# Optimization experiments

Hardware: AMD Instinct MI355X
Metric: run time of the kernel (lower is better)

Reference implementation:

```python
import jax, jax.numpy as jnp
import numpy as np

B, T, TF = 4, 16000, 80
NC, NR, NS, NO, NIN, NL = 80, 64, 256, 256, 256, 16
K_UP, STRIDE = 800, 200
LOOP_FACTOR = 8  # floor(log2(128)) + 1


def setup_inputs() -> dict:
    key = jax.random.key(0)
    ks = jax.random.split(key, 16)
    s = 0.05
    return {
        "features": jax.random.normal(ks[0], (B, NC, TF), jnp.float32),
        "forward_input": jax.random.randint(ks[1], (B, T), 0, NIN, jnp.int32),
        "embed_table": jax.random.normal(ks[2], (NIN, NR), jnp.float32) * s,
        "up_w": jax.random.normal(ks[3], (NC, NC, K_UP), jnp.float32) * s,  # torch ConvTranspose1d (in,out,K)
        "up_b": jnp.zeros((NC,), jnp.float32),
        "cond_w": jax.random.normal(ks[4], (2 * NR * NL, NC), jnp.float32) * s,
        "cond_b": jnp.zeros((2 * NR * NL,), jnp.float32),
        "dil_w": jax.random.normal(ks[5], (NL, 2 * NR, NR, 2), jnp.float32) * s,
        "dil_b": jnp.zeros((NL, 2 * NR), jnp.float32),
        "res_w": jax.random.normal(ks[6], (NL - 1, NR, NR), jnp.float32) * s,
        "res_b": jnp.zeros((NL - 1, NR), jnp.float32),
        "skip_w": jax.random.normal(ks[7], (NL, NS, NR), jnp.float32) * s,
        "skip_b": jnp.zeros((NL, NS), jnp.float32),
        "out_w": jax.random.normal(ks[8], (NO, NS), jnp.float32) * s,
        "end_w": jax.random.normal(ks[9], (NO, NO), jnp.float32) * s,
    }


def reference(features, forward_input, embed_table, up_w, up_b, cond_w, cond_b,
              dil_w, dil_b, res_w, res_b, skip_w, skip_b, out_w, end_w):
    # ConvTranspose1d(stride=200): conv with lhs_dilation, spatially-flipped kernel, in/out swapped
    k_t = jnp.flip(up_w, -1).transpose(1, 0, 2)  # (out, in, K)
    cond = jax.lax.conv_general_dilated(
        features, k_t, window_strides=(1,), padding=[(K_UP - 1, K_UP - 1)],
        lhs_dilation=(STRIDE,), dimension_numbers=('NCH', 'OIH', 'NCH'))
    cond = cond + up_b[None, :, None]
    cond = cond[:, :, :T]  # truncate to signal length

    x = embed_table[forward_input].transpose(0, 2, 1)  # [B, NR, T]

    cond_acts = jnp.einsum('oc,bct->bot', cond_w, cond) + cond_b[None, :, None]
    cond_acts = cond_acts.reshape(B, NL, 2 * NR, T)

    res_acts = None
    output = None
    for i in range(NL):
        d = 2 ** (i % LOOP_FACTOR)
        prev = jnp.pad(x, ((0, 0), (0, 0), (d, 0)))[:, :, :T]  # causal shift by dilation
        in_act = (jnp.einsum('oi,bit->bot', dil_w[i, :, :, 0], prev)
                  + jnp.einsum('oi,bit->bot', dil_w[i, :, :, 1], x)
                  + dil_b[i][None, :, None] + cond_acts[:, i])
        acts = jnp.tanh(in_act[:, :NR]) * jax.nn.sigmoid(in_act[:, NR:])
        if i < NL - 1:
            res_acts = jnp.einsum('oi,bit->bot', res_w[i], acts) + res_b[i][None, :, None]
        # NOTE: faithful to original: on last layer res_acts is stale (from layer NL-2)
        x = res_acts + x
        skip = jnp.einsum('oi,bit->bot', skip_w[i], acts) + skip_b[i][None, :, None]
        output = skip if output is None else output + skip

    output = jax.nn.relu(output)
    output = jax.nn.relu(jnp.einsum('os,bst->bot', out_w, output))
    output = jnp.einsum('oi,bit->bot', end_w, output)
    # shift right by one, zero-fill first frame
    output = jnp.concatenate([jnp.zeros_like(output[:, :, :1]), output[:, :, :-1]], axis=2)
    return output
```

## Files before the change

kernel.cpp:

```cpp
#include <hip/hip_runtime.h>
#include <hip/hip_bf16.h>

#define TT 16000
#define BB 4
#define NLAYER 16
#define NBLK 1000
#define BARSTR 1088
#define BARSZ (15 * BARSTR)
#define XCSTR 72
#define XPSTR 72
#define ACSTR 72
#define CDSTR 88
#define M3STR 264
#define ABSTR 72

#define A1SZ (NLAYER*8*7*512)
#define A2SZ (NLAYER*4*2*512)
#define SWSZ (16*32*512)
#define OWSZ (16*8*512)
#define AUPSZ (20*10*512)
#define BUPSZ (1000*10*512)

typedef unsigned short ushort_t;
typedef unsigned long long u64_t;
typedef short v8s __attribute__((ext_vector_type(8)));
typedef short v4s __attribute__((ext_vector_type(4)));
typedef float v4f __attribute__((ext_vector_type(4)));

#define MFMA16 __builtin_amdgcn_mfma_f32_16x16x32_bf16

__device__ __forceinline__ float bf2f(ushort_t u) {
  unsigned int x = ((unsigned int)u) << 16;
  float f; __builtin_memcpy(&f, &x, 4); return f;
}
__device__ __forceinline__ ushort_t f2bf(float f) {
  unsigned int x; __builtin_memcpy(&x, &f, 4);
  x += 0x7fffu + ((x >> 16) & 1u);
  return (ushort_t)(x >> 16);
}

__global__ __launch_bounds__(256) void kprep(
    const float* __restrict__ feat, const int* __restrict__ fin,
    const float* __restrict__ embed, const float* __restrict__ up_w,
    const float* __restrict__ cond_w, const float* __restrict__ cond_b,
    const float* __restrict__ dil_w, const float* __restrict__ dil_b,
    const float* __restrict__ res_w, const float* __restrict__ skip_w,
    const float* __restrict__ skip_b, const float* __restrict__ out_w,
    const float* __restrict__ end_w,
    ushort_t* __restrict__ A1, ushort_t* __restrict__ A2,
    ushort_t* __restrict__ SWf, ushort_t* __restrict__ OWf,
    ushort_t* __restrict__ EWf, ushort_t* __restrict__ Aup,
    ushort_t* __restrict__ Bup, ushort_t* __restrict__ x0,
    float* __restrict__ Bcomb, float* __restrict__ SBsum,
    unsigned int* __restrict__ bar) {
  int tid = blockIdx.x * 256 + threadIdx.x;
  int np = gridDim.x * 256;
  for (int idx = tid; idx < BARSZ; idx += np) bar[idx] = 0u;
  for (int idx = tid; idx < A1SZ; idx += np) {
    int j = idx & 7, lane = (idx >> 3) & 63;
    int r_ = idx >> 9;
    int ks = r_ % 7; int r2 = r_ / 7;
    int mt = r2 & 7; int i = r2 >> 3;
    int m = mt * 16 + (lane & 15);
    int k = ks * 32 + (lane >> 4) * 8 + j;
    float v = 0.f;
    if (k < 64)       v = dil_w[((i * 128 + m) * 64 + k) * 2 + 1];
    else if (k < 128) v = dil_w[((i * 128 + m) * 64 + (k - 64)) * 2 + 0];
    else if (k < 208) v = cond_w[(i * 128 + m) * 80 + (k - 128)];
    A1[idx] = f2bf(v);
  }
  for (int idx = tid; idx < A2SZ; idx += np) {
    int j = idx & 7, lane = (idx >> 3) & 63;
    int r_ = idx >> 9;
    int ks = r_ & 1; int mt = (r_ >> 1) & 3; int i = r_ >> 3;
    int m = mt * 16 + (lane & 15);
    int k = ks * 32 + (lane >> 4) * 8 + j;
    A2[idx] = f2bf(i < 15 ? res_w[(i * 64 + m) * 64 + k] : 0.f);
  }
  for (int idx = tid; idx < SWSZ; idx += np) {
    int j = idx & 7, lane = (idx >> 3) & 63;
    int r_ = idx >> 9;
    int ks = r_ & 31; int mt = r_ >> 5;
    int m = mt * 16 + (lane & 15);
    int k = ks * 32 + (lane >> 4) * 8 + j;
    int i = k >> 6, ch = k & 63;
    SWf[idx] = f2bf(skip_w[(i * 256 + m) * 64 + ch]);
  }
  for (int idx = tid; idx < OWSZ; idx += np) {
    int j = idx & 7, lane = (idx >> 3) & 63;
    int r_ = idx >> 9;
    int ks = r_ & 7; int mt = r_ >> 3;
    int m = mt * 16 + (lane & 15);
    int k = ks * 32 + (lane >> 4) * 8 + j;
    OWf[idx] = f2bf(out_w[m * 256 + k]);
    EWf[idx] = f2bf(end_w[m * 256 + k]);
  }
  for (int idx = tid; idx < AUPSZ; idx += np) {
    int j = idx & 7, lane = (idx >> 3) & 63;
    int r_ = idx >> 9;
    int ks = r_ % 10; int mt = r_ / 10;
    int mrow = mt * 16 + (lane & 15);
    int km = ks * 32 + (lane >> 4) * 8 + j;
    int b = mrow / 80, q = mrow % 80;
    int m = km / 80, i = km % 80;
    int jj = q - m;
    Aup[idx] = f2bf(jj >= 0 ? feat[(b * 80 + i) * 80 + jj] : 0.f);
  }
  for (int idx = tid; idx < BUPSZ; idx += np) {
    int j = idx & 7, lane = (idx >> 3) & 63;
    int r_ = idx >> 9;
    int ks = r_ % 10; int nt = r_ / 10;
    int km = ks * 32 + (lane >> 4) * 8 + j;
    int m = km / 80, i = km % 80;
    int col = nt * 16 + (lane & 15);
    int o = col / 200, r = col % 200;
    Bup[idx] = f2bf(up_w[(size_t)(i * 80 + o) * 800 + m * 200 + r]);
  }
  for (int idx = tid; idx < BB * TT * 64; idx += np) {
    int k = idx & 63;
    int bt = idx >> 6;
    x0[idx] = f2bf(embed[fin[bt] * 64 + k]);
  }
  for (int idx = tid; idx < NLAYER * 128; idx += np)
    Bcomb[idx] = dil_b[idx] + cond_b[idx];
  for (int idx = tid; idx < 256; idx += np) {
    float s = 0.f;
    for (int i = 0; i < NLAYER; i++) s += skip_b[i * 256 + idx];
    SBsum[idx] = s;
  }
}

__global__ __launch_bounds__(256) void kup(
    const ushort_t* __restrict__ Aup, const ushort_t* __restrict__ Bup,
    const float* __restrict__ up_b, ushort_t* __restrict__ cond) {
  int nt0 = blockIdx.x * 4;
  int lane = threadIdx.x & 63;
  int w = threadIdx.x >> 6;
  int tl = lane & 15, quad = lane >> 4;
  v4f acc[5][4];
  #pragma unroll
  for (int mt = 0; mt < 5; mt++)
    #pragma unroll
    for (int nt = 0; nt < 4; nt++) acc[mt][nt] = 0.f;
  #pragma unroll
  for (int ks = 0; ks < 10; ks++) {
    v8s bf[4];
    #pragma unroll
    for (int nt = 0; nt < 4; nt++)
      bf[nt] = *(const v8s*)(Bup + (((size_t)(nt0 + nt) * 10 + ks) * 64 + lane) * 8);
    #pragma unroll
    for (int mt = 0; mt < 5; mt++) {
      v8s a = *(const v8s*)(Aup + (((size_t)(w * 5 + mt) * 10 + ks) * 64 + lane) * 8);
      #pragma unroll
      for (int nt = 0; nt < 4; nt++)
        acc[mt][nt] = MFMA16(a, bf[nt], acc[mt][nt], 0, 0, 0);
    }
  }
  #pragma unroll
  for (int mt = 0; mt < 5; mt++) {
    #pragma unroll
    for (int nt = 0; nt < 4; nt++) {
      int col = (nt0 + nt) * 16 + tl;
      int o = col / 200, r = col % 200;
      float bias = up_b[o];
      #pragma unroll
      for (int rg = 0; rg < 4; rg++) {
        int mrow = (w * 5 + mt) * 16 + quad * 4 + rg;
        int b = mrow / 80, q = mrow % 80;
        cond[((size_t)b * TT + q * 200 + r) * 80 + o] = f2bf(acc[mt][nt][rg] + bias);
      }
    }
  }
}

__global__ __launch_bounds__(256, 4) void kchain(
    ushort_t* __restrict__ x0g, ushort_t* __restrict__ x1g,
    const ushort_t* __restrict__ cond, ushort_t* __restrict__ actsb,
    const ushort_t* __restrict__ A1, const ushort_t* __restrict__ A2,
    const float* __restrict__ Bcomb, const float* __restrict__ resb,
    unsigned int* __restrict__ bar) {
  __shared__ ushort_t Uxc[64 * XCSTR];
  __shared__ ushort_t Uhalo[64 * XPSTR];
  __shared__ ushort_t Uact[64 * ACSTR];
  __shared__ ushort_t Ucd[64 * CDSTR + 8];
  int b = blockIdx.y;
  int t0 = blockIdx.x * 64;
  int tidx = threadIdx.x;
  int lane = tidx & 63;
  int w = tidx >> 6;
  int tl = lane & 15, quad = lane >> 4;
  int cha = w * 16 + quad * 4;
  const size_t lstr = (size_t)BB * TT * 64;

  const ushort_t* xb0 = x0g + ((size_t)b * TT + t0) * 64;
  for (int e = tidx * 8; e < 4096; e += 2048) {
    int t = e >> 6, c = e & 63;
    *(v8s*)&Uxc[t * XCSTR + c] = *(const v8s*)(xb0 + e);
  }
  const ushort_t* cbp = cond + ((size_t)b * TT + t0) * 80;
  for (int e = tidx * 8; e < 5120; e += 2048) {
    int t = e / 80, c = e - t * 80;
    *(v8s*)&Ucd[t * CDSTR + c] = *(const v8s*)(cbp + e);
  }
  for (int e2 = tidx; e2 < 520; e2 += 256) {
    if (e2 < 512) Ucd[(e2 >> 3) * CDSTR + 80 + (e2 & 7)] = 0;
    else          Ucd[64 * CDSTR + (e2 - 512)] = 0;
  }
  __syncthreads();

  for (int l = 0; l < NLAYER; l++) {
    int d = 1 << (l & 7);
    int hr = (d < 64) ? d : 64;
    const ushort_t* xing = (l & 1) ? x1g : x0g;
    ushort_t* xoutg = (l & 1) ? x0g : x1g;
    const ushort_t* A1l = A1 + (size_t)l * 8 * 7 * 512;
    const ushort_t* A2l = A2 + (size_t)l * 4 * 2 * 512;
    const float* Bb = Bcomb + l * 128;
    const float* rb = resb + (l < 15 ? l : 0) * 64;
    int last = (l == NLAYER - 1);

    for (int e = tidx * 8; e < hr * 64; e += 2048) {
      int t = e >> 6, c = e & 63;
      int tp = t0 + t - d;
      v8s v = (v8s)0;
      if (tp >= 0) {
        const u64_t* p = (const u64_t*)(xing + ((size_t)b * TT + tp) * 64 + c);
        u64_t w0 = __hip_atomic_load(p, __ATOMIC_RELAXED, __HIP_MEMORY_SCOPE_AGENT);
        u64_t w1 = __hip_atomic_load(p + 1, __ATOMIC_RELAXED, __HIP_MEMORY_SCOPE_AGENT);
        __builtin_memcpy(&v, &w0, 8);
        __builtin_memcpy(((char*)&v) + 8, &w1, 8);
      }
      *(v8s*)&Uhalo[t * XPSTR + c] = v;
    }
    __syncthreads();

    v4f acc0[4], acc1[4];
    #pragma unroll
    for (int nt = 0; nt < 4; nt++) { acc0[nt] = 0.f; acc1[nt] = 0.f; }
    #pragma unroll
    for (int ks = 0; ks < 7; ks++) {
      v8s a0 = *(const v8s*)(A1l + (((size_t)w * 7 + ks) * 64 + lane) * 8);
      v8s a1 = *(const v8s*)(A1l + (((size_t)(w + 4) * 7 + ks) * 64 + lane) * 8);
      #pragma unroll
      for (int nt = 0; nt < 4; nt++) {
        int t = nt * 16 + tl;
        const ushort_t* bp;
        if (ks < 2) {
          bp = &Uxc[t * XCSTR + ks * 32 + quad * 8];
        } else if (ks < 4) {
          int toff = t - d;
          bp = (toff >= 0) ? &Uxc[toff * XCSTR + (ks - 2) * 32 + quad * 8]
                           : &Uhalo[t * XPSTR + (ks - 2) * 32 + quad * 8];
        } else {
          bp = &Ucd[t * CDSTR + (ks - 4) * 32 + quad * 8];
        }
        v8s bf = *(const v8s*)bp;
        acc0[nt] = MFMA16(a0, bf, acc0[nt], 0, 0, 0);
        acc1[nt] = MFMA16(a1, bf, acc1[nt], 0, 0, 0);
      }
    }

    float ba[4], bb_[4];
    #pragma unroll
    for (int r = 0; r < 4; r++) { ba[r] = Bb[cha + r]; bb_[r] = Bb[64 + cha + r]; }
    #pragma unroll
    for (int nt = 0; nt < 4; nt++) {
      int t = nt * 16 + tl;
      v4s pk;
      #pragma unroll
      for (int r = 0; r < 4; r++) {
        float ia = acc0[nt][r] + ba[r];
        float ib = acc1[nt][r] + bb_[r];
        float ax = fabsf(ia);
        float e2 = __expf(-2.f * ax);
        float th = __builtin_copysignf((1.f - e2) / (1.f + e2), ia);
        float sg = 1.f / (1.f + __expf(-ib));
        pk[r] = (short)f2bf(th * sg);
      }
      *(v4s*)&Uact[t * ACSTR + cha] = pk;
    }
    __syncthreads();

    ushort_t* ab = actsb + (size_t)l * lstr + ((size_t)b * TT + t0) * 64;
    for (int e = tidx * 8; e < 4096; e += 2048) {
      int t = e >> 6, c = e & 63;
      *(v8s*)(ab + e) = *(const v8s*)&Uact[t * ACSTR + c];
    }

    if (!last) {
      v4f acc2[4];
      #pragma unroll
      for (int nt = 0; nt < 4; nt++) {
        v4f z;
        #pragma unroll
        for (int r = 0; r < 4; r++) z[r] = rb[cha + r];
        acc2[nt] = z;
      }
      #pragma unroll
      for (int ks = 0; ks < 2; ks++) {
        v8s a = *(const v8s*)(A2l + (((size_t)w * 2 + ks) * 64 + lane) * 8);
        #pragma unroll
        for (int nt = 0; nt < 4; nt++) {
          v8s bf = *(const v8s*)&Uact[(nt * 16 + tl) * ACSTR + ks * 32 + quad * 8];
          acc2[nt] = MFMA16(a, bf, acc2[nt], 0, 0, 0);
        }
      }
      #pragma unroll
      for (int nt = 0; nt < 4; nt++) {
        int t = nt * 16 + tl;
        v4s xo = *(const v4s*)&Uxc[t * XCSTR + cha];
        v4s nw;
        #pragma unroll
        for (int r = 0; r < 4; r++)
          nw[r] = (short)f2bf(acc2[nt][r] + bf2f((ushort_t)xo[r]));
        *(v4s*)&Uxc[t * XCSTR + cha] = nw;
      }
      __syncthreads();

      int dnext = 1 << ((l + 1) & 7);
      int tmin = 64 - (dnext < 64 ? dnext : 64);
      ushort_t* xob = xoutg + ((size_t)b * TT + t0) * 64;
      for (int e = tidx * 8; e < 4096; e += 2048) {
        int t = e >> 6, c = e & 63;
        if (t >= tmin) {
          v8s v = *(const v8s*)&Uxc[t * XCSTR + c];
          u64_t w0, w1;
          __builtin_memcpy(&w0, &v, 8);
          __builtin_memcpy(&w1, ((const char*)&v) + 8, 8);
          u64_t* p = (u64_t*)(xob + e);
          __hip_atomic_store(p, w0, __ATOMIC_RELAXED, __HIP_MEMORY_SCOPE_AGENT);
          __hip_atomic_store(p + 1, w1, __ATOMIC_RELAXED, __HIP_MEMORY_SCOPE_AGENT);
        }
      }

      __syncthreads();
      if (tidx == 0) {
        unsigned int* L = bar + l * BARSTR;
        int flat = b * 250 + blockIdx.x;
        int shard = flat & 15;
        unsigned int tgt = (shard < 8) ? 62u : 61u;
        unsigned int old = __hip_atomic_fetch_add(L + shard * 32, 1u,
            __ATOMIC_RELAXED, __HIP_MEMORY_SCOPE_AGENT);
        if (old == tgt) {
          unsigned int ro = __hip_atomic_fetch_add(L + 16 * 32, 1u,
              __ATOMIC_RELAXED, __HIP_MEMORY_SCOPE_AGENT);
          if (ro == 15u) {
            #pragma unroll
            for (int s = 0; s < 16; s++)
              __hip_atomic_store(L + (17 + s) * 32, 1u,
                  __ATOMIC_RELAXED, __HIP_MEMORY_SCOPE_AGENT);
          }
        }
        while (__hip_atomic_load(L + (17 + shard) * 32,
            __ATOMIC_RELAXED, __HIP_MEMORY_SCOPE_AGENT) == 0u)
          __builtin_amdgcn_s_sleep(16);
      }
      __syncthreads();
    }
  }
}

#define KF_COMPUTE(L, BUF)                                                    \
  {                                                                           \
    _Pragma("unroll")                                                         \
    for (int ks2 = 0; ks2 < 2; ks2++) {                                       \
      int ksg = (L) * 2 + ks2;                                                \
      v8s bf[4];                                                              \
      _Pragma("unroll")                                                       \
      for (int nt = 0; nt < 4; nt++)                                          \
        bf[nt] = *(const v8s*)&(BUF)[(nt * 16 + tl) * ABSTR + ks2 * 32 +      \
                                     quad * 8];                               \
      _Pragma("unroll")                                                       \
      for (int mt = 0; mt < 4; mt++) {                                        \
        v8s a = *(const v8s*)(SWf +                                           \
            (((size_t)(w * 4 + mt) * 32 + ksg) * 64 + lane) * 8);             \
        _Pragma("unroll")                                                     \
        for (int nt = 0; nt < 4; nt++)                                        \
          acc[mt][nt] = MFMA16(a, bf[nt], acc[mt][nt], 0, 0, 0);              \
      }                                                                       \
    }                                                                         \
  }

__global__ __launch_bounds__(256) void kfinal(
    const ushort_t* __restrict__ actsb,
    const ushort_t* __restrict__ SWf, const ushort_t* __restrict__ OWf,
    const ushort_t* __restrict__ EWf, const float* __restrict__ SBsum,
    float* __restrict__ dout) {
  __shared__ ushort_t SMEM[64 * M3STR];
  int b = blockIdx.y;
  int t0 = blockIdx.x * 64;
  int tidx = threadIdx.x;
  int lane = tidx & 63;
  int w = tidx >> 6;
  int tl = lane & 15, quad = lane >> 4;

  v4f acc[4][4];
  #pragma unroll
  for (int mt = 0; mt < 4; mt++) {
    int o = (w * 4 + mt) * 16 + quad * 4;
    #pragma unroll
    for (int nt = 0; nt < 4; nt++) {
      v4f z;
      #pragma unroll
      for (int r = 0; r < 4; r++) z[r] = SBsum[o + r];
      acc[mt][nt] = z;
    }
  }
  const size_t lstr = (size_t)BB * TT * 64;
  int tq = tidx >> 2;
  int pq = (tidx & 3) * 16;
  const ushort_t* a0p = actsb + ((size_t)b * TT + t0) * 64 + tq * 64 + pq;
  {
    v8s p0 = *(const v8s*)(a0p);
    v8s p1 = *(const v8s*)(a0p + 8);
    *(v8s*)&SMEM[tq * ABSTR + pq] = p0;
    *(v8s*)&SMEM[tq * ABSTR + pq + 8] = p1;
  }
  v8s qa0 = *(const v8s*)(a0p + 1 * lstr);
  v8s qa1 = *(const v8s*)(a0p + 1 * lstr + 8);
  v8s qb0 = *(const v8s*)(a0p + 2 * lstr);
  v8s qb1 = *(const v8s*)(a0p + 2 * lstr + 8);
  __syncthreads();
  for (int l = 0; l < NLAYER; l += 2) {
    KF_COMPUTE(l, SMEM);
    *(v8s*)&SMEM[64 * ABSTR + tq * ABSTR + pq] = qa0;
    *(v8s*)&SMEM[64 * ABSTR + tq * ABSTR + pq + 8] = qa1;
    {
      int ln = (l + 3 < NLAYER) ? (l + 3) : (NLAYER - 1);
      qa0 = *(const v8s*)(a0p + (size_t)ln * lstr);
      qa1 = *(const v8s*)(a0p + (size_t)ln * lstr + 8);
    }
    __syncthreads();
    KF_COMPUTE(l + 1, SMEM + 64 * ABSTR);
    *(v8s*)&SMEM[tq * ABSTR + pq] = qb0;
    *(v8s*)&SMEM[tq * ABSTR + pq + 8] = qb1;
    {
      int ln = (l + 4 < NLAYER) ? (l + 4) : (NLAYER - 1);
      qb0 = *(const v8s*)(a0p + (size_t)ln * lstr);
      qb1 = *(const v8s*)(a0p + (size_t)ln * lstr + 8);
    }
    __syncthreads();
  }
  #pragma unroll
  for (int mt = 0; mt < 4; mt++) {
    int o = (w * 4 + mt) * 16 + quad * 4;
    #pragma unroll
    for (int nt = 0; nt < 4; nt++) {
      int t = nt * 16 + tl;
      #pragma unroll
      for (int r = 0; r < 4; r++)
        SMEM[t * M3STR + o + r] = f2bf(fmaxf(acc[mt][nt][r], 0.f));
    }
  }
  __syncthreads();

  v4f acc2[4][4];
  #pragma unroll
  for (int mt = 0; mt < 4; mt++)
    #pragma unroll
    for (int nt = 0; nt < 4; nt++) acc2[mt][nt] = 0.f;
  #pragma unroll
  for (int ks = 0; ks < 8; ks++) {
    v8s bf[4];
    #pragma unroll
    for (int nt = 0; nt < 4; nt++)
      bf[nt] = *(const v8s*)&SMEM[(nt * 16 + tl) * M3STR + ks * 32 + quad * 8];
    #pragma unroll
    for (int mt = 0; mt < 4; mt++) {
      v8s a = *(const v8s*)(OWf + (((size_t)(w * 4 + mt) * 8 + ks) * 64 + lane) * 8);
      #pragma unroll
      for (int nt = 0; nt < 4; nt++)
        acc2[mt][nt] = MFMA16(a, bf[nt], acc2[mt][nt], 0, 0, 0);
    }
  }
  __syncthreads();
  #pragma unroll
  for (int mt = 0; mt < 4; mt++) {
    int o = (w * 4 + mt) * 16 + quad * 4;
    #pragma unroll
    for (int nt = 0; nt < 4; nt++) {
      int t = nt * 16 + tl;
      #pragma unroll
      for (int r = 0; r < 4; r++)
        SMEM[t * M3STR + o + r] = f2bf(fmaxf(acc2[mt][nt][r], 0.f));
    }
  }
  __syncthreads();

  v4f acc3[4][4];
  #pragma unroll
  for (int mt = 0; mt < 4; mt++)
    #pragma unroll
    for (int nt = 0; nt < 4; nt++) acc3[mt][nt] = 0.f;
  #pragma unroll
  for (int ks = 0; ks < 8; ks++) {
    v8s bf[4];
    #pragma unroll
    for (int nt = 0; nt < 4; nt++)
      bf[nt] = *(const v8s*)&SMEM[(nt * 16 + tl) * M3STR + ks * 32 + quad * 8];
    #pragma unroll
    for (int mt = 0; mt < 4; mt++) {
      v8s a = *(const v8s*)(EWf + (((size_t)(w * 4 + mt) * 8 + ks) * 64 + lane) * 8);
      #pragma unroll
      for (int nt = 0; nt < 4; nt++)
        acc3[mt][nt] = MFMA16(a, bf[nt], acc3[mt][nt], 0, 0, 0);
    }
  }
  #pragma unroll
  for (int mt = 0; mt < 4; mt++) {
    #pragma unroll
    for (int nt = 0; nt < 4; nt++) {
      int tg = t0 + nt * 16 + tl;
      #pragma unroll
      for (int r = 0; r < 4; r++) {
        int o = (w * 4 + mt) * 16 + quad * 4 + r;
        float* ob = dout + ((size_t)b * 256 + o) * TT;
        if (tg == 0) ob[0] = 0.f;
        if (tg + 1 < TT) ob[tg + 1] = acc3[mt][nt][r];
      }
    }
  }
}

extern "C" void kernel_launch(void* const* d_in, const int* in_sizes, int n_in,
                              void* d_out, int out_size, void* d_ws, size_t ws_size,
                              hipStream_t stream) {
  const float* feat   = (const float*)d_in[0];
  const int*   fin    = (const int*)d_in[1];
  const float* embed  = (const float*)d_in[2];
  const float* up_w   = (const float*)d_in[3];
  const float* up_b   = (const float*)d_in[4];
  const float* cond_w = (const float*)d_in[5];
  const float* cond_b = (const float*)d_in[6];
  const float* dil_w  = (const float*)d_in[7];
  const float* dil_b  = (const float*)d_in[8];
  const float* res_w  = (const float*)d_in[9];
  const float* res_b  = (const float*)d_in[10];
  const float* skip_w = (const float*)d_in[11];
  const float* skip_b = (const float*)d_in[12];
  const float* out_w  = (const float*)d_in[13];
  const float* end_w  = (const float*)d_in[14];

  float* ws = (float*)d_ws;
  unsigned int* bar = (unsigned int*)ws;
  size_t off = BARSZ;
  float* Bcomb = ws + off; off += NLAYER * 128;
  float* SBsum = ws + off; off += 256;
  ushort_t* ub = (ushort_t*)(ws + off);
  size_t uo = 0;
  ushort_t* A1   = ub + uo; uo += A1SZ;
  ushort_t* A2   = ub + uo; uo += A2SZ;
  ushort_t* SWf  = ub + uo; uo += SWSZ;
  ushort_t* OWf  = ub + uo; uo += OWSZ;
  ushort_t* EWf  = ub + uo; uo += OWSZ;
  ushort_t* Aup  = ub + uo; uo += AUPSZ;
  ushort_t* Bup  = ub + uo; uo += BUPSZ;
  ushort_t* cond = ub + uo; uo += (size_t)BB * TT * 80;
  ushort_t* x0   = ub + uo; uo += (size_t)BB * TT * 64;
  ushort_t* x1   = ub + uo; uo += (size_t)BB * TT * 64;
  ushort_t* acts = ub + uo; uo += (size_t)NLAYER * BB * TT * 64;

  kprep<<<1024, 256, 0, stream>>>(feat, fin, embed, up_w, cond_w, cond_b,
      dil_w, dil_b, res_w, skip_w, skip_b, out_w, end_w,
      A1, A2, SWf, OWf, EWf, Aup, Bup, x0, Bcomb, SBsum, bar);
  kup<<<250, 256, 0, stream>>>(Aup, Bup, up_b, cond);
  kchain<<<dim3(250, BB), 256, 0, stream>>>(x0, x1, cond, acts,
      A1, A2, Bcomb, res_b, bar);
  kfinal<<<dim3(250, BB), 256, 0, stream>>>(acts, SWf, OWf, EWf, SBsum,
      (float*)d_out);
}
```

Before: 431.4 us.

## Transpose cond layout, merge halo/act LDS buffers, use nontemporal acts traffic

The upsampling kernel now writes cond channel-major ([B][80][T]), so its scattered stores along time become contiguous. The chain kernel transposes cond into LDS with scalar loads. The halo and activation LDS buffers are merged into one, with an extra barrier, to cut shared memory so the occupancy hint can rise from 4 to 5. The large acts tensor is written and read with nontemporal hints to avoid polluting the caches. The trade-offs are an extra barrier per layer and narrower, less vectorised cond loads into LDS.

```diff
diff --git a/kernel.cpp b/kernel.cpp
--- a/kernel.cpp
+++ b/kernel.cpp
@@ -132,7 +132,7 @@
 
 __global__ __launch_bounds__(256) void kup(
     const ushort_t* __restrict__ Aup, const ushort_t* __restrict__ Bup,
-    const float* __restrict__ up_b, ushort_t* __restrict__ cond) {
+    const float* __restrict__ up_b, ushort_t* __restrict__ condT) {
   int nt0 = blockIdx.x * 4;
   int lane = threadIdx.x & 63;
   int w = threadIdx.x >> 6;
@@ -167,21 +167,21 @@
       for (int rg = 0; rg < 4; rg++) {
         int mrow = (w * 5 + mt) * 16 + quad * 4 + rg;
         int b = mrow / 80, q = mrow % 80;
-        cond[((size_t)b * TT + q * 200 + r) * 80 + o] = f2bf(acc[mt][nt][rg] + bias);
-      }
-    }
-  }
-}
-
-__global__ __launch_bounds__(256, 4) void kchain(
+        condT[((size_t)b * 80 + o) * TT + q * 200 + r] =
+            f2bf(acc[mt][nt][rg] + bias);
+      }
+    }
+  }
+}
+
+__global__ __launch_bounds__(256, 5) void kchain(
     ushort_t* __restrict__ x0g, ushort_t* __restrict__ x1g,
-    const ushort_t* __restrict__ cond, ushort_t* __restrict__ actsb,
+    const ushort_t* __restrict__ condT, ushort_t* __restrict__ actsb,
     const ushort_t* __restrict__ A1, const ushort_t* __restrict__ A2,
     const float* __restrict__ Bcomb, const float* __restrict__ resb,
     unsigned int* __restrict__ bar) {
   __shared__ ushort_t Uxc[64 * XCSTR];
-  __shared__ ushort_t Uhalo[64 * XPSTR];
-  __shared__ ushort_t Uact[64 * ACSTR];
+  __shared__ ushort_t UhAct[64 * XPSTR];
   __shared__ ushort_t Ucd[64 * CDSTR + 8];
   int b = blockIdx.y;
   int t0 = blockIdx.x * 64;
@@ -197,10 +197,9 @@
     int t = e >> 6, c = e & 63;
     *(v8s*)&Uxc[t * XCSTR + c] = *(const v8s*)(xb0 + e);
   }
-  const ushort_t* cbp = cond + ((size_t)b * TT + t0) * 80;
-  for (int e = tidx * 8; e < 5120; e += 2048) {
-    int t = e / 80, c = e - t * 80;
-    *(v8s*)&Ucd[t * CDSTR + c] = *(const v8s*)(cbp + e);
+  for (int e = tidx; e < 5120; e += 256) {
+    int c = e >> 6, t = e & 63;
+    Ucd[t * CDSTR + c] = condT[((size_t)b * 80 + c) * TT + t0 + t];
   }
   for (int e2 = tidx; e2 < 520; e2 += 256) {
     if (e2 < 512) Ucd[(e2 >> 3) * CDSTR + 80 + (e2 & 7)] = 0;
@@ -230,7 +229,7 @@
         __builtin_memcpy(&v, &w0, 8);
         __builtin_memcpy(((char*)&v) + 8, &w1, 8);
       }
-      *(v8s*)&Uhalo[t * XPSTR + c] = v;
+      *(v8s*)&UhAct[t * XPSTR + c] = v;
     }
     __syncthreads();
 
@@ -250,7 +249,7 @@
         } else if (ks < 4) {
           int toff = t - d;
           bp = (toff >= 0) ? &Uxc[toff * XCSTR + (ks - 2) * 32 + quad * 8]
-                           : &Uhalo[t * XPSTR + (ks - 2) * 32 + quad * 8];
+                           : &UhAct[t * XPSTR + (ks - 2) * 32 + quad * 8];
         } else {
           bp = &Ucd[t * CDSTR + (ks - 4) * 32 + quad * 8];
         }
@@ -259,6 +258,7 @@
         acc1[nt] = MFMA16(a1, bf, acc1[nt], 0, 0, 0);
       }
     }
+    __syncthreads();
 
     float ba[4], bb_[4];
     #pragma unroll
@@ -277,14 +277,15 @@
         float sg = 1.f / (1.f + __expf(-ib));
         pk[r] = (short)f2bf(th * sg);
       }
-      *(v4s*)&Uact[t * ACSTR + cha] = pk;
+      *(v4s*)&UhAct[t * ACSTR + cha] = pk;
     }
     __syncthreads();
 
     ushort_t* ab = actsb + (size_t)l * lstr + ((size_t)b * TT + t0) * 64;
     for (int e = tidx * 8; e < 4096; e += 2048) {
       int t = e >> 6, c = e & 63;
-      *(v8s*)(ab + e) = *(const v8s*)&Uact[t * ACSTR + c];
+      v8s v = *(const v8s*)&UhAct[t * ACSTR + c];
+      __builtin_nontemporal_store(v, (v8s*)(ab + e));
     }
 
     if (!last) {
@@ -301,7 +302,7 @@
         v8s a = *(const v8s*)(A2l + (((size_t)w * 2 + ks) * 64 + lane) * 8);
         #pragma unroll
         for (int nt = 0; nt < 4; nt++) {
-          v8s bf = *(const v8s*)&Uact[(nt * 16 + tl) * ACSTR + ks * 32 + quad * 8];
+          v8s bf = *(const v8s*)&UhAct[(nt * 16 + tl) * ACSTR + ks * 32 + quad * 8];
           acc2[nt] = MFMA16(a, bf, acc2[nt], 0, 0, 0);
         }
       }
@@ -411,15 +412,15 @@
   int pq = (tidx & 3) * 16;
   const ushort_t* a0p = actsb + ((size_t)b * TT + t0) * 64 + tq * 64 + pq;
   {
-    v8s p0 = *(const v8s*)(a0p);
-    v8s p1 = *(const v8s*)(a0p + 8);
+    v8s p0 = __builtin_nontemporal_load((const v8s*)(a0p));
+    v8s p1 = __builtin_nontemporal_load((const v8s*)(a0p + 8));
     *(v8s*)&SMEM[tq * ABSTR + pq] = p0;
     *(v8s*)&SMEM[tq * ABSTR + pq + 8] = p1;
   }
-  v8s qa0 = *(const v8s*)(a0p + 1 * lstr);
-  v8s qa1 = *(const v8s*)(a0p + 1 * lstr + 8);
-  v8s qb0 = *(const v8s*)(a0p + 2 * lstr);
-  v8s qb1 = *(const v8s*)(a0p + 2 * lstr + 8);
+  v8s qa0 = __builtin_nontemporal_load((const v8s*)(a0p + 1 * lstr));
+  v8s qa1 = __builtin_nontemporal_load((const v8s*)(a0p + 1 * lstr + 8));
+  v8s qb0 = __builtin_nontemporal_load((const v8s*)(a0p + 2 * lstr));
+  v8s qb1 = __builtin_nontemporal_load((const v8s*)(a0p + 2 * lstr + 8));
   __syncthreads();
   for (int l = 0; l < NLAYER; l += 2) {
     KF_COMPUTE(l, SMEM);
@@ -427,8 +428,8 @@
     *(v8s*)&SMEM[64 * ABSTR + tq * ABSTR + pq + 8] = qa1;
     {
       int ln = (l + 3 < NLAYER) ? (l + 3) : (NLAYER - 1);
-      qa0 = *(const v8s*)(a0p + (size_t)ln * lstr);
-      qa1 = *(const v8s*)(a0p + (size_t)ln * lstr + 8);
+      qa0 = __builtin_nontemporal_load((const v8s*)(a0p + (size_t)ln * lstr));
+      qa1 = __builtin_nontemporal_load((const v8s*)(a0p + (size_t)ln * lstr + 8));
     }
     __syncthreads();
     KF_COMPUTE(l + 1, SMEM + 64 * ABSTR);
@@ -436,8 +437,8 @@
     *(v8s*)&SMEM[tq * ABSTR + pq + 8] = qb1;
     {
       int ln = (l + 4 < NLAYER) ? (l + 4) : (NLAYER - 1);
-      qb0 = *(const v8s*)(a0p + (size_t)ln * lstr);
-      qb1 = *(const v8s*)(a0p + (size_t)ln * lstr + 8);
+      qb0 = __builtin_nontemporal_load((const v8s*)(a0p + (size_t)ln * lstr));
+      qb1 = __builtin_nontemporal_load((const v8s*)(a0p + (size_t)ln * lstr + 8));
     }
     __syncthreads();
   }
@@ -548,23 +549,23 @@
   float* SBsum = ws + off; off += 256;
   ushort_t* ub = (ushort_t*)(ws + off);
   size_t uo = 0;
-  ushort_t* A1   = ub + uo; uo += A1SZ;
-  ushort_t* A2   = ub + uo; uo += A2SZ;
-  ushort_t* SWf  = ub + uo; uo += SWSZ;
-  ushort_t* OWf  = ub + uo; uo += OWSZ;
-  ushort_t* EWf  = ub + uo; uo += OWSZ;
-  ushort_t* Aup  = ub + uo; uo += AUPSZ;
-  ushort_t* Bup  = ub + uo; uo += BUPSZ;
-  ushort_t* cond = ub + uo; uo += (size_t)BB * TT * 80;
-  ushort_t* x0   = ub + uo; uo += (size_t)BB * TT * 64;
-  ushort_t* x1   = ub + uo; uo += (size_t)BB * TT * 64;
-  ushort_t* acts = ub + uo; uo += (size_t)NLAYER * BB * TT * 64;
+  ushort_t* A1    = ub + uo; uo += A1SZ;
+  ushort_t* A2    = ub + uo; uo += A2SZ;
+  ushort_t* SWf   = ub + uo; uo += SWSZ;
+  ushort_t* OWf   = ub + uo; uo += OWSZ;
+  ushort_t* EWf   = ub + uo; uo += OWSZ;
+  ushort_t* Aup   = ub + uo; uo += AUPSZ;
+  ushort_t* Bup   = ub + uo; uo += BUPSZ;
+  ushort_t* condT = ub + uo; uo += (size_t)BB * 80 * TT;
+  ushort_t* x0    = ub + uo; uo += (size_t)BB * TT * 64;
+  ushort_t* x1    = ub + uo; uo += (size_t)BB * TT * 64;
+  ushort_t* acts  = ub + uo; uo += (size_t)NLAYER * BB * TT * 64;
 
   kprep<<<1024, 256, 0, stream>>>(feat, fin, embed, up_w, cond_w, cond_b,
       dil_w, dil_b, res_w, skip_w, skip_b, out_w, end_w,
       A1, A2, SWf, OWf, EWf, Aup, Bup, x0, Bcomb, SBsum, bar);
-  kup<<<250, 256, 0, stream>>>(Aup, Bup, up_b, cond);
-  kchain<<<dim3(250, BB), 256, 0, stream>>>(x0, x1, cond, acts,
+  kup<<<250, 256, 0, stream>>>(Aup, Bup, up_b, condT);
+  kchain<<<dim3(250, BB), 256, 0, stream>>>(x0, x1, condT, acts,
       A1, A2, Bcomb, res_b, bar);
   kfinal<<<dim3(250, BB), 256, 0, stream>>>(acts, SWf, OWf, EWf, SBsum,
       (float*)d_out);
```

New measurement: 415.0 us. 3.8% less time.
